# Performance work log

Hardware: AMD Instinct MI355X
Metric: run time of the kernel (lower is better)

## Reference

```python
import jax, jax.numpy as jnp
import numpy as np

P = 0.1        # error_prob
VOCAB = 128    # vocab_size
B, L = 64, 4096

def setup_inputs() -> dict:
    key = jax.random.key(0)
    k1, k2, k3 = jax.random.split(key, 3)
    message = jax.random.uniform(k1, (B, L, VOCAB), dtype=jnp.float32)
    rand_u = jax.random.uniform(k2, (B, L), dtype=jnp.float32)
    # torch.randint(high=vocab_size - 2) -> values in [0, VOCAB-2)
    replacement_indices = jax.random.randint(k3, (B, L), 0, VOCAB - 2, dtype=jnp.int32)
    return {"message": message, "rand_u": rand_u,
            "replacement_indices": replacement_indices}

def reference(message, rand_u, replacement_indices):
    # message: [B, L, V] float distribution over symbols (3D branch of forward)
    msg = jnp.argmax(message, axis=-1)                 # [B, L] int
    target_ids = rand_u < P                            # positions to corrupt
    # Excluded-category sampling via offset-shift: candidates are
    # [1 .. V-1] with msg_exp removed (V-2 candidates). Candidate at index r
    # equals r+1, shifted by one if it would collide with the excluded symbol.
    msg_exp = jnp.where(msg != 0, msg, 1)
    r1 = replacement_indices + 1
    replacement_symbols = r1 + (r1 >= msg_exp).astype(replacement_indices.dtype)
    not_eos = msg != 0
    combined = jnp.logical_and(target_ids, not_eos)    # [B, L]
    replaced_probs = jax.nn.one_hot(replacement_symbols, VOCAB,
                                    dtype=message.dtype)  # [B, L, V]
    return jnp.where(combined[:, :, None], replaced_probs, message)
```

## Files before the change

### kernel.cpp

```cpp
#include <hip/hip_runtime.h>


constexpr int V = 128;
constexpr float P = 0.1f;

typedef float f4 __attribute__((ext_vector_type(4)));

__global__ __launch_bounds__(256) void SymmetricChannel_kernel(
    const float* __restrict__ msg,
    const float* __restrict__ rand_u,
    const int*   __restrict__ rep_idx,
    float*       __restrict__ out,
    int n_rows)
{
    int tid    = blockIdx.x * blockDim.x + threadIdx.x;
    int row    = tid >> 5;
    int lane32 = tid & 31;
    if (row >= n_rows) return;

    const f4* mrow = (const f4*)(msg + (size_t)row * V);
    f4 v = __builtin_nontemporal_load(mrow + lane32);

    float ru = rand_u[row];
    f4 o = v;

    if (ru < P) {
        float best = v.x; int bidx = 0;
        if (v.y > best) { best = v.y; bidx = 1; }
        if (v.z > best) { best = v.z; bidx = 2; }
        if (v.w > best) { best = v.w; bidx = 3; }
        int gidx = lane32 * 4 + bidx;

        #pragma unroll
        for (int m = 16; m > 0; m >>= 1) {
            float ov = __shfl_xor(best, m, 32);
            int   oi = __shfl_xor(gidx, m, 32);
            if (ov > best || (ov == best && oi < gidx)) { best = ov; gidx = oi; }
        }

        int am = gidx;
        if (am != 0) {
            int r1  = rep_idx[row] + 1;
            int sym = r1 + (r1 >= am ? 1 : 0);
            int base = lane32 * 4;
            o.x = (base + 0 == sym) ? 1.0f : 0.0f;
            o.y = (base + 1 == sym) ? 1.0f : 0.0f;
            o.z = (base + 2 == sym) ? 1.0f : 0.0f;
            o.w = (base + 3 == sym) ? 1.0f : 0.0f;
        }
    }

    __builtin_nontemporal_store(o, (f4*)(out + (size_t)row * V) + lane32);
}

extern "C" void kernel_launch(void* const* d_in, const int* in_sizes, int n_in,
                              void* d_out, int out_size, void* d_ws, size_t ws_size,
                              hipStream_t stream) {
    const float* msg = (const float*)d_in[0];
    const float* ru  = (const float*)d_in[1];
    const int*   ri  = (const int*)d_in[2];
    float* out = (float*)d_out;

    int n_rows = in_sizes[1];
    int threads = 256;
    long long total = (long long)n_rows * 32;
    int blocks = (int)((total + threads - 1) / threads);
    SymmetricChannel_kernel<<<blocks, threads, 0, stream>>>(msg, ru, ri, out, n_rows);
}
```

Baseline: 222.2 us.

## Use persistent grid-stride loop with two rows in flight per thread

Caps the grid at 2048 blocks and makes each thread loop over the work with a grid stride, loading two rows' float4 slices before computing and storing them. The aim is to cut block launch overhead and overlap two independent memory loads per thread. The trade-off is fewer resident waves overall, which could leave less memory parallelism than launching the full grid.

```diff
diff --git a/kernel.cpp b/kernel.cpp
--- a/kernel.cpp
+++ b/kernel.cpp
@@ -11,46 +11,58 @@
     const float* __restrict__ rand_u,
     const int*   __restrict__ rep_idx,
     float*       __restrict__ out,
-    int n_rows)
+    long long total)
 {
-    int tid    = blockIdx.x * blockDim.x + threadIdx.x;
-    int row    = tid >> 5;
-    int lane32 = tid & 31;
-    if (row >= n_rows) return;
+    const long long stride = (long long)gridDim.x * blockDim.x;
+    const long long tid    = (long long)blockIdx.x * blockDim.x + threadIdx.x;
+    const int lane32 = threadIdx.x & 31;
+    const int base   = lane32 * 4;
 
-    const f4* mrow = (const f4*)(msg + (size_t)row * V);
-    f4 v = __builtin_nontemporal_load(mrow + lane32);
+    auto compute = [&](f4 v, float ru, long long row) -> f4 {
+        f4 o = v;
+        if (ru < P) {
+            float best = v.x; int bidx = 0;
+            if (v.y > best) { best = v.y; bidx = 1; }
+            if (v.z > best) { best = v.z; bidx = 2; }
+            if (v.w > best) { best = v.w; bidx = 3; }
+            int gidx = base + bidx;
+            #pragma unroll
+            for (int m = 16; m > 0; m >>= 1) {
+                float ov = __shfl_xor(best, m, 32);
+                int   oi = __shfl_xor(gidx, m, 32);
+                if (ov > best || (ov == best && oi < gidx)) { best = ov; gidx = oi; }
+            }
+            int am = gidx;
+            if (am != 0) {
+                int r1  = rep_idx[row] + 1;
+                int sym = r1 + (r1 >= am ? 1 : 0);
+                o.x = (base + 0 == sym) ? 1.0f : 0.0f;
+                o.y = (base + 1 == sym) ? 1.0f : 0.0f;
+                o.z = (base + 2 == sym) ? 1.0f : 0.0f;
+                o.w = (base + 3 == sym) ? 1.0f : 0.0f;
+            }
+        }
+        return o;
+    };
 
-    float ru = rand_u[row];
-    f4 o = v;
+    for (long long s = tid; s < total; s += 2 * stride) {
+        long long sB   = s + stride;
+        bool hasB      = sB < total;
+        long long rowA = s >> 5;
+        long long rowB = hasB ? (sB >> 5) : rowA;
 
-    if (ru < P) {
-        float best = v.x; int bidx = 0;
-        if (v.y > best) { best = v.y; bidx = 1; }
-        if (v.z > best) { best = v.z; bidx = 2; }
-        if (v.w > best) { best = v.w; bidx = 3; }
-        int gidx = lane32 * 4 + bidx;
+        f4 vA = __builtin_nontemporal_load((const f4*)(msg + rowA * V) + lane32);
+        f4 vB = __builtin_nontemporal_load((const f4*)(msg + rowB * V) + lane32);
+        float ruA = rand_u[rowA];
+        float ruB = rand_u[rowB];
 
-        #pragma unroll
-        for (int m = 16; m > 0; m >>= 1) {
-            float ov = __shfl_xor(best, m, 32);
-            int   oi = __shfl_xor(gidx, m, 32);
-            if (ov > best || (ov == best && oi < gidx)) { best = ov; gidx = oi; }
-        }
-
-        int am = gidx;
-        if (am != 0) {
-            int r1  = rep_idx[row] + 1;
-            int sym = r1 + (r1 >= am ? 1 : 0);
-            int base = lane32 * 4;
-            o.x = (base + 0 == sym) ? 1.0f : 0.0f;
-            o.y = (base + 1 == sym) ? 1.0f : 0.0f;
-            o.z = (base + 2 == sym) ? 1.0f : 0.0f;
-            o.w = (base + 3 == sym) ? 1.0f : 0.0f;
+        f4 oA = compute(vA, ruA, rowA);
+        __builtin_nontemporal_store(oA, (f4*)(out + rowA * V) + lane32);
+        if (hasB) {
+            f4 oB = compute(vB, ruB, rowB);
+            __builtin_nontemporal_store(oB, (f4*)(out + rowB * V) + lane32);
         }
     }
-
-    __builtin_nontemporal_store(o, (f4*)(out + (size_t)row * V) + lane32);
 }
 
 extern "C" void kernel_launch(void* const* d_in, const int* in_sizes, int n_in,
@@ -61,9 +73,10 @@
     const int*   ri  = (const int*)d_in[2];
     float* out = (float*)d_out;
 
-    int n_rows = in_sizes[1];
+    long long n_rows = in_sizes[1];
+    long long total  = n_rows * 32;
     int threads = 256;
-    long long total = (long long)n_rows * 32;
-    int blocks = (int)((total + threads - 1) / threads);
-    SymmetricChannel_kernel<<<blocks, threads, 0, stream>>>(msg, ru, ri, out, n_rows);
+    long long want = (total + threads - 1) / threads;
+    int blocks = (int)(want < 2048 ? want : 2048);
+    SymmetricChannel_kernel<<<blocks, threads, 0, stream>>>(msg, ru, ri, out, total);
 }
```

Result: slower. 231.2 us (+4.0%).
